# Performance work log

Hardware: AMD Instinct MI355X
Metric: run time of the kernel (lower is better)

## Reference

```python
import jax, jax.numpy as jnp
import numpy as np

H = 4096      # hidden_size
F = 14336     # intermediate_size (ffn)
GS = 64       # HQQ group_size along axis 0 (output rows)
NB = 4        # nbits
T = 512       # tokens routed to this expert


def _make_qlinear(key, N, K):
    """Quantized weight of logical shape (N, K) = (out, in), HQQ axis=0 groups."""
    k1, k2, k3 = jax.random.split(key, 3)
    W_q = jax.random.randint(k1, (N, K), 0, 2 ** NB, dtype=jnp.int32)
    scale = jax.random.uniform(k2, (N // GS, K), dtype=jnp.float32) * 0.02 + 1e-3
    zero = jax.random.uniform(k3, (N // GS, K), dtype=jnp.float32) * (2.0 ** (NB - 1))
    return W_q, scale, zero


def setup_inputs() -> dict:
    key = jax.random.key(0)
    kx, k1, k2, k3 = jax.random.split(key, 4)
    w1_q, w1_scale, w1_zero = _make_qlinear(k1, F, H)  # gate proj
    w2_q, w2_scale, w2_zero = _make_qlinear(k2, H, F)  # down proj
    w3_q, w3_scale, w3_zero = _make_qlinear(k3, F, H)  # up proj
    hidden_states = jax.random.normal(kx, (T, H), dtype=jnp.float32)
    return dict(hidden_states=hidden_states,
                w1_q=w1_q, w1_scale=w1_scale, w1_zero=w1_zero,
                w2_q=w2_q, w2_scale=w2_scale, w2_zero=w2_zero,
                w3_q=w3_q, w3_scale=w3_scale, w3_zero=w3_zero)


def _dequant(W_q, scale, zero):
    # W[n, k] = (W_q[n, k] - zero[n // GS, k]) * scale[n // GS, k]
    N, K = W_q.shape
    Wf = W_q.reshape(N // GS, GS, K).astype(scale.dtype)
    return ((Wf - zero[:, None, :]) * scale[:, None, :]).reshape(N, K)


def reference(hidden_states,
              w1_q, w1_scale, w1_zero,
              w2_q, w2_scale, w2_zero,
              w3_q, w3_scale, w3_zero):
    gate = hidden_states @ _dequant(w1_q, w1_scale, w1_zero).T  # [T, F]
    up = hidden_states @ _dequant(w3_q, w3_scale, w3_zero).T    # [T, F]
    inter = jax.nn.silu(gate) * up                               # [T, F]
    return inter @ _dequant(w2_q, w2_scale, w2_zero).T           # [T, H]
```

## Files before the change

kernel.cpp:

```cpp
#include <hip/hip_runtime.h>
#include <stdint.h>

typedef __bf16 bf16;
typedef __attribute__((ext_vector_type(8))) bf16 bf16x8;
typedef __attribute__((ext_vector_type(4))) bf16 bf16x4;
typedef __attribute__((ext_vector_type(4))) float f32x4;

#define T_DIM 512
#define H_DIM 4096
#define F_DIM 14336

__device__ __forceinline__ int swz(int r, int c) {
    return r * 64 + (c ^ ((r & 7) << 3));
}

__device__ __forceinline__ int xcd_remap(int d, int chunk) {
    return (d & 7) * chunk + (d >> 3);
}

__device__ __forceinline__ void dma16(const void* g, void* l) {
    __builtin_amdgcn_global_load_lds(
        (const __attribute__((address_space(1))) void*)g,
        (__attribute__((address_space(3))) void*)l, 16, 0, 0);
}

#define BARRIER_VM(N)                                                        \
    {                                                                        \
        __builtin_amdgcn_sched_barrier(0);                                   \
        asm volatile("s_waitcnt vmcnt(" #N ") lgkmcnt(0)\n\ts_barrier" ::: "memory"); \
        __builtin_amdgcn_sched_barrier(0);                                   \
    }

__global__ void cvt_x_kernel(const float* __restrict__ x, bf16* __restrict__ xbt) {
    int i = (blockIdx.x * 256 + threadIdx.x) * 4;
    int m = i >> 12;
    int c = i & 4095;
    float4 v = *(const float4*)(x + i);
    bf16x4 o = {(bf16)v.x, (bf16)v.y, (bf16)v.z, (bf16)v.w};
    int p = m >> 7, rm = m & 127, kt = c >> 6, kc = c & 63;
    *(bf16x4*)(xbt + (size_t)(p * 64 + kt) * 8192 + swz(rm, kc)) = o;
}

struct WSet { int4 q1[2], q3[2]; float4 s1, z1, s3, z3; };

__global__ __launch_bounds__(256, 3)
void gemm_gateup(const bf16* __restrict__ A,
                 const int* __restrict__ Wq1, const float* __restrict__ Sc1,
                 const float* __restrict__ Zr1,
                 const int* __restrict__ Wq3, const float* __restrict__ Sc3,
                 const float* __restrict__ Zr3,
                 bf16* __restrict__ inter) {
    constexpr int KD = H_DIM;
    constexpr int NT = KD / 64;
    __shared__ __align__(16) bf16 As[2][128 * 64];
    __shared__ __align__(16) bf16 Bs1[2][32 * 64];
    __shared__ __align__(16) bf16 Bs3[2][32 * 64];

    const int l    = xcd_remap(blockIdx.x, 224);
    const int bx   = l & 3;
    const int by   = l >> 2;
    const int tid  = threadIdx.x;
    const int lane = tid & 63;
    const int wid  = tid >> 6;
    const int wm   = wid >> 1, wn = wid & 1;
    const int lr   = lane & 15;
    const int lk   = (lane >> 4) * 8;
    const int m0   = bx * 128;
    const int n0   = by * 32;
    const int grp  = n0 >> 6;

    const int b_r = (tid >> 4) * 2;
    const int b_c = (tid & 15) * 4;

    const char*  atile = (const char*)A + (size_t)bx * 64 * 16384;
    const size_t dmaoff = (size_t)wid * 4096 + lane * 16;

    const int*   q1B = Wq1 + (size_t)(n0 + b_r) * KD + b_c;
    const int*   q3B = Wq3 + (size_t)(n0 + b_r) * KD + b_c;
    const float* s1B = Sc1 + (size_t)grp * KD + b_c;
    const float* z1B = Zr1 + (size_t)grp * KD + b_c;
    const float* s3B = Sc3 + (size_t)grp * KD + b_c;
    const float* z3B = Zr3 + (size_t)grp * KD + b_c;

    f32x4 acc1[4], acc3[4];
    const f32x4 zf = {0.f, 0.f, 0.f, 0.f};
#pragma unroll
    for (int i = 0; i < 4; i++) { acc1[i] = zf; acc3[i] = zf; }

    WSet sA, sB;

#define GU_DMA(TILE, nb)                                                      \
    {                                                                         \
        const char* _s = atile + (size_t)(TILE) * 16384 + dmaoff;             \
        char* _d = (char*)&As[nb][0] + wid * 4096;                            \
        _Pragma("unroll")                                                     \
        for (int j = 0; j < 4; j++) dma16(_s + j * 1024, _d + j * 1024);      \
    }

#define GU_STAGE(S, K0)                                                       \
    {                                                                         \
        _Pragma("unroll")                                                     \
        for (int i = 0; i < 2; i++) {                                         \
            S.q1[i] = *(const int4*)(q1B + (size_t)i * KD + (K0));            \
            S.q3[i] = *(const int4*)(q3B + (size_t)i * KD + (K0));            \
        }                                                                     \
        S.s1 = *(const float4*)(s1B + (K0));                                  \
        S.z1 = *(const float4*)(z1B + (K0));                                  \
        S.s3 = *(const float4*)(s3B + (K0));                                  \
        S.z3 = *(const float4*)(z3B + (K0));                                  \
    }

#define GU_WLDS(S, nb)                                                        \
    {                                                                         \
        float4 n1, n3;                                                        \
        n1.x = -S.z1.x * S.s1.x; n1.y = -S.z1.y * S.s1.y;                     \
        n1.z = -S.z1.z * S.s1.z; n1.w = -S.z1.w * S.s1.w;                     \
        n3.x = -S.z3.x * S.s3.x; n3.y = -S.z3.y * S.s3.y;                     \
        n3.z = -S.z3.z * S.s3.z; n3.w = -S.z3.w * S.s3.w;                     \
        _Pragma("unroll")                                                     \
        for (int i = 0; i < 2; i++) {                                         \
            bf16x4 v;                                                         \
            v[0] = (bf16)fmaf((float)S.q1[i].x, S.s1.x, n1.x);                \
            v[1] = (bf16)fmaf((float)S.q1[i].y, S.s1.y, n1.y);                \
            v[2] = (bf16)fmaf((float)S.q1[i].z, S.s1.z, n1.z);                \
            v[3] = (bf16)fmaf((float)S.q1[i].w, S.s1.w, n1.w);                \
            *(bf16x4*)&Bs1[nb][swz(b_r + i, b_c)] = v;                        \
            bf16x4 u;                                                         \
            u[0] = (bf16)fmaf((float)S.q3[i].x, S.s3.x, n3.x);                \
            u[1] = (bf16)fmaf((float)S.q3[i].y, S.s3.y, n3.y);                \
            u[2] = (bf16)fmaf((float)S.q3[i].z, S.s3.z, n3.z);                \
            u[3] = (bf16)fmaf((float)S.q3[i].w, S.s3.w, n3.w);                \
            *(bf16x4*)&Bs3[nb][swz(b_r + i, b_c)] = u;                        \
        }                                                                     \
    }

#define GU_MFMA(nb)                                                           \
    {                                                                         \
        _Pragma("unroll")                                                     \
        for (int kk = 0; kk < 2; kk++) {                                      \
            bf16x8 af[4], b1, b3;                                             \
            _Pragma("unroll")                                                 \
            for (int mi = 0; mi < 4; mi++)                                    \
                af[mi] = *(const bf16x8*)&As[nb][swz(wm * 64 + mi * 16 + lr, kk * 32 + lk)]; \
            b1 = *(const bf16x8*)&Bs1[nb][swz(wn * 16 + lr, kk * 32 + lk)];   \
            b3 = *(const bf16x8*)&Bs3[nb][swz(wn * 16 + lr, kk * 32 + lk)];   \
            _Pragma("unroll")                                                 \
            for (int mi = 0; mi < 4; mi++) {                                  \
                acc1[mi] = __builtin_amdgcn_mfma_f32_16x16x32_bf16(af[mi], b1, acc1[mi], 0, 0, 0); \
                acc3[mi] = __builtin_amdgcn_mfma_f32_16x16x32_bf16(af[mi], b3, acc3[mi], 0, 0, 0); \
            }                                                                 \
        }                                                                     \
    }

    GU_STAGE(sA, 0);
    GU_DMA(0, 0);
    GU_WLDS(sA, 0);
    GU_STAGE(sB, 64);
    GU_STAGE(sA, 128);
    BARRIER_VM(16);

    for (int t = 0; t < NT; t += 2) {
        if (t + 1 < NT) GU_DMA(t + 1, 1);
        __builtin_amdgcn_sched_barrier(0);
        GU_MFMA(0);
        if (t + 1 < NT) {
            GU_WLDS(sB, 1);
            if (t + 3 < NT) {
                GU_STAGE(sB, (t + 3) * 64);
                BARRIER_VM(8);
            } else {
                BARRIER_VM(0);
            }
        }
        const int u = t + 1;
        if (u < NT) {
            if (u + 1 < NT) GU_DMA(u + 1, 0);
            __builtin_amdgcn_sched_barrier(0);
            GU_MFMA(1);
            if (u + 1 < NT) {
                GU_WLDS(sA, 0);
                if (u + 3 < NT) {
                    GU_STAGE(sA, (u + 3) * 64);
                    BARRIER_VM(8);
                } else {
                    BARRIER_VM(0);
                }
            }
        }
    }
#undef GU_DMA
#undef GU_STAGE
#undef GU_WLDS
#undef GU_MFMA

    const int orow = (lane >> 4) * 4;
    const int cg   = n0 + wn * 16 + lr;
    const int kt   = cg >> 6, kc = cg & 63;
    bf16* itile = inter + (size_t)(bx * 224 + kt) * 8192;
#pragma unroll
    for (int mi = 0; mi < 4; mi++) {
#pragma unroll
        for (int r = 0; r < 4; r++) {
            int rm = (wm * 64 + mi * 16 + orow + r) & 127;
            float g = acc1[mi][r];
            float u = acc3[mi][r];
            float s = g / (1.0f + __expf(-g));
            itile[swz(rm, kc)] = (bf16)(s * u);
        }
    }
}

struct WSetD { int4 q[2]; float4 s, z; };

template<int SPLITK>
__global__ __launch_bounds__(256, 4)
void gemm_down(const bf16* __restrict__ A,
               const int* __restrict__ Wq,
               const float* __restrict__ Sc, const float* __restrict__ Zr,
               float* __restrict__ partials) {
    constexpr int KD = F_DIM;
    constexpr int KC = KD / SPLITK;
    constexpr int NT = KC / 64;
    __shared__ __align__(16) bf16 As[2][128 * 64];
    __shared__ __align__(16) bf16 Bs[2][32 * 64];

    const int l    = xcd_remap(blockIdx.x, 64 * SPLITK);
    const int bx   = l & 3;
    const int by   = (l >> 2) & 127;
    const int bz   = l >> 9;
    const int tid  = threadIdx.x;
    const int lane = tid & 63;
    const int wid  = tid >> 6;
    const int wm   = wid >> 1, wn = wid & 1;
    const int lr   = lane & 15;
    const int lk   = (lane >> 4) * 8;
    const int m0   = bx * 128;
    const int n0   = by * 32;
    const int grp  = n0 >> 6;
    const int kt0  = bz * (KC / 64);

    const int b_r = (tid >> 4) * 2;
    const int b_c = (tid & 15) * 4;

    const char*  atile = (const char*)A + (size_t)(bx * 224 + kt0) * 16384;
    const size_t dmaoff = (size_t)wid * 4096 + lane * 16;
    const int    kbeg  = bz * KC;

    const int*   qB = Wq + (size_t)(n0 + b_r) * KD + kbeg + b_c;
    const float* sB_ = Sc + (size_t)grp * KD + kbeg + b_c;
    const float* zB_ = Zr + (size_t)grp * KD + kbeg + b_c;

    f32x4 acc[4];
    const f32x4 zf = {0.f, 0.f, 0.f, 0.f};
#pragma unroll
    for (int i = 0; i < 4; i++) acc[i] = zf;

    WSetD sA, sB;

#define GD_DMA(TILE, nb)                                                      \
    {                                                                         \
        const char* _s = atile + (size_t)(TILE) * 16384 + dmaoff;             \
        char* _d = (char*)&As[nb][0] + wid * 4096;                            \
        _Pragma("unroll")                                                     \
        for (int j = 0; j < 4; j++) dma16(_s + j * 1024, _d + j * 1024);      \
    }

#define GD_STAGE(S, K0)                                                       \
    {                                                                         \
        _Pragma("unroll")                                                     \
        for (int i = 0; i < 2; i++)                                           \
            S.q[i] = *(const int4*)(qB + (size_t)i * KD + (K0));              \
        S.s = *(const float4*)(sB_ + (K0));                                   \
        S.z = *(const float4*)(zB_ + (K0));                                   \
    }

#define GD_WLDS(S, nb)                                                        \
    {                                                                         \
        float4 nz;                                                            \
        nz.x = -S.z.x * S.s.x; nz.y = -S.z.y * S.s.y;                         \
        nz.z = -S.z.z * S.s.z; nz.w = -S.z.w * S.s.w;                         \
        _Pragma("unroll")                                                     \
        for (int i = 0; i < 2; i++) {                                         \
            bf16x4 v;                                                         \
            v[0] = (bf16)fmaf((float)S.q[i].x, S.s.x, nz.x);                  \
            v[1] = (bf16)fmaf((float)S.q[i].y, S.s.y, nz.y);                  \
            v[2] = (bf16)fmaf((float)S.q[i].z, S.s.z, nz.z);                  \
            v[3] = (bf16)fmaf((float)S.q[i].w, S.s.w, nz.w);                  \
            *(bf16x4*)&Bs[nb][swz(b_r + i, b_c)] = v;                         \
        }                                                                     \
    }

#define GD_MFMA(nb)                                                           \
    {                                                                         \
        _Pragma("unroll")                                                     \
        for (int kk = 0; kk < 2; kk++) {                                      \
            bf16x8 af[4], bfr;                                                \
            _Pragma("unroll")                                                 \
            for (int mi = 0; mi < 4; mi++)                                    \
                af[mi] = *(const bf16x8*)&As[nb][swz(wm * 64 + mi * 16 + lr, kk * 32 + lk)]; \
            bfr = *(const bf16x8*)&Bs[nb][swz(wn * 16 + lr, kk * 32 + lk)];   \
            _Pragma("unroll")                                                 \
            for (int mi = 0; mi < 4; mi++)                                    \
                acc[mi] = __builtin_amdgcn_mfma_f32_16x16x32_bf16(af[mi], bfr, acc[mi], 0, 0, 0); \
        }                                                                     \
    }

    GD_STAGE(sA, 0);
    GD_DMA(0, 0);
    GD_WLDS(sA, 0);
    GD_STAGE(sB, 64);
    GD_STAGE(sA, 128);
    BARRIER_VM(8);

    for (int t = 0; t < NT; t += 2) {
        if (t + 1 < NT) GD_DMA(t + 1, 1);
        __builtin_amdgcn_sched_barrier(0);
        GD_MFMA(0);
        if (t + 1 < NT) {
            GD_WLDS(sB, 1);
            if (t + 3 < NT) {
                GD_STAGE(sB, (t + 3) * 64);
                BARRIER_VM(4);
            } else {
                BARRIER_VM(0);
            }
        }
        const int u = t + 1;
        if (u < NT) {
            if (u + 1 < NT) GD_DMA(u + 1, 0);
            __builtin_amdgcn_sched_barrier(0);
            GD_MFMA(1);
            if (u + 1 < NT) {
                GD_WLDS(sA, 0);
                if (u + 3 < NT) {
                    GD_STAGE(sA, (u + 3) * 64);
                    BARRIER_VM(4);
                } else {
                    BARRIER_VM(0);
                }
            }
        }
    }
#undef GD_DMA
#undef GD_STAGE
#undef GD_WLDS
#undef GD_MFMA

    float* po = partials + (size_t)bz * T_DIM * H_DIM;
    const int orow = (lane >> 4) * 4;
#pragma unroll
    for (int mi = 0; mi < 4; mi++) {
#pragma unroll
        for (int r = 0; r < 4; r++) {
            int m = m0 + wm * 64 + mi * 16 + orow + r;
            int c = n0 + wn * 16 + lr;
            po[(size_t)m * H_DIM + c] = acc[mi][r];
        }
    }
}

template<int S>
__global__ void reduce_kernel(const float* __restrict__ partials, float* __restrict__ out) {
    size_t i = ((size_t)blockIdx.x * 256 + threadIdx.x) * 4;
    f32x4 a = *(const f32x4*)(partials + i);
#pragma unroll
    for (int s = 1; s < S; s++)
        a += *(const f32x4*)(partials + (size_t)s * T_DIM * H_DIM + i);
    *(f32x4*)(out + i) = a;
}

extern "C" void kernel_launch(void* const* d_in, const int* in_sizes, int n_in,
                              void* d_out, int out_size, void* d_ws, size_t ws_size,
                              hipStream_t stream) {
    const float* x   = (const float*)d_in[0];
    const int*   w1q = (const int*)d_in[1];
    const float* w1s = (const float*)d_in[2];
    const float* w1z = (const float*)d_in[3];
    const int*   w2q = (const int*)d_in[4];
    const float* w2s = (const float*)d_in[5];
    const float* w2z = (const float*)d_in[6];
    const int*   w3q = (const int*)d_in[7];
    const float* w3s = (const float*)d_in[8];
    const float* w3z = (const float*)d_in[9];

    bf16*  xb    = (bf16*)d_ws;
    bf16*  inter = xb + (size_t)T_DIM * H_DIM;
    float* parts = (float*)(inter + (size_t)T_DIM * F_DIM);

    const size_t base   = (size_t)T_DIM * H_DIM * 2 + (size_t)T_DIM * F_DIM * 2;
    const size_t pbytes = (size_t)T_DIM * H_DIM * 4;

    cvt_x_kernel<<<dim3(2048), dim3(256), 0, stream>>>(x, xb);

    gemm_gateup<<<dim3(1792), dim3(256), 0, stream>>>(
        xb, w1q, w1s, w1z, w3q, w3s, w3z, inter);

    if (ws_size >= base + 4 * pbytes) {
        gemm_down<4><<<dim3(2048), dim3(256), 0, stream>>>(inter, w2q, w2s, w2z, parts);
        reduce_kernel<4><<<dim3(2048), dim3(256), 0, stream>>>(parts, (float*)d_out);
    } else if (ws_size >= base + 2 * pbytes) {
        gemm_down<2><<<dim3(1024), dim3(256), 0, stream>>>(inter, w2q, w2s, w2z, parts);
        reduce_kernel<2><<<dim3(2048), dim3(256), 0, stream>>>(parts, (float*)d_out);
    } else {
        gemm_down<1><<<dim3(512), dim3(256), 0, stream>>>(inter, w2q, w2s, w2z, parts);
        reduce_kernel<1><<<dim3(2048), dim3(256), 0, stream>>>(parts, (float*)d_out);
    }
}
```

Baseline: 453.7 us.

## Load gate/up operands directly into registers, dropping LDS staging and barriers

The gate/up GEMM stops staging activations and dequantized weights in shared memory. Each wave now reads its A fragments straight from the pre-swizzled global bf16 tile and dequantizes its own int4 weight fragment in registers, which removes the LDS round trip and the block barriers. Tiles change to a 64x64 N block per block with 16 columns per wave, and launch bounds drop to 2 blocks per SM. In exchange, A is re-read from global/L2 by every wave with no sharing, register pressure rises, and occupancy falls.

```diff
diff --git a/kernel.cpp b/kernel.cpp
--- a/kernel.cpp
+++ b/kernel.cpp
@@ -30,6 +30,20 @@
         asm volatile("s_waitcnt vmcnt(" #N ") lgkmcnt(0)\n\ts_barrier" ::: "memory"); \
         __builtin_amdgcn_sched_barrier(0);                                   \
     }
+
+__device__ __forceinline__ bf16x8 deq8(int4 qa, int4 qb, float4 sa, float4 sb,
+                                       float4 za, float4 zb) {
+    bf16x8 r;
+    r[0] = (bf16)(((float)qa.x - za.x) * sa.x);
+    r[1] = (bf16)(((float)qa.y - za.y) * sa.y);
+    r[2] = (bf16)(((float)qa.z - za.z) * sa.z);
+    r[3] = (bf16)(((float)qa.w - za.w) * sa.w);
+    r[4] = (bf16)(((float)qb.x - zb.x) * sb.x);
+    r[5] = (bf16)(((float)qb.y - zb.y) * sb.y);
+    r[6] = (bf16)(((float)qb.z - zb.z) * sb.z);
+    r[7] = (bf16)(((float)qb.w - zb.w) * sb.w);
+    return r;
+}
 
 __global__ void cvt_x_kernel(const float* __restrict__ x, bf16* __restrict__ xbt) {
     int i = (blockIdx.x * 256 + threadIdx.x) * 4;
@@ -41,9 +55,9 @@
     *(bf16x4*)(xbt + (size_t)(p * 64 + kt) * 8192 + swz(rm, kc)) = o;
 }
 
-struct WSet { int4 q1[2], q3[2]; float4 s1, z1, s3, z3; };
-
-__global__ __launch_bounds__(256, 3)
+struct QSet { int4 q1[4], q3[4]; };
+
+__global__ __launch_bounds__(256, 2)
 void gemm_gateup(const bf16* __restrict__ A,
                  const int* __restrict__ Wq1, const float* __restrict__ Sc1,
                  const float* __restrict__ Zr1,
@@ -52,160 +66,121 @@
                  bf16* __restrict__ inter) {
     constexpr int KD = H_DIM;
     constexpr int NT = KD / 64;
-    __shared__ __align__(16) bf16 As[2][128 * 64];
-    __shared__ __align__(16) bf16 Bs1[2][32 * 64];
-    __shared__ __align__(16) bf16 Bs3[2][32 * 64];
 
     const int l    = xcd_remap(blockIdx.x, 224);
-    const int bx   = l & 3;
-    const int by   = l >> 2;
+    const int mp   = l & 7;
+    const int np   = l >> 3;
     const int tid  = threadIdx.x;
     const int lane = tid & 63;
-    const int wid  = tid >> 6;
-    const int wm   = wid >> 1, wn = wid & 1;
+    const int w    = tid >> 6;
     const int lr   = lane & 15;
     const int lk   = (lane >> 4) * 8;
-    const int m0   = bx * 128;
-    const int n0   = by * 32;
-    const int grp  = n0 >> 6;
-
-    const int b_r = (tid >> 4) * 2;
-    const int b_c = (tid & 15) * 4;
-
-    const char*  atile = (const char*)A + (size_t)bx * 64 * 16384;
-    const size_t dmaoff = (size_t)wid * 4096 + lane * 16;
-
-    const int*   q1B = Wq1 + (size_t)(n0 + b_r) * KD + b_c;
-    const int*   q3B = Wq3 + (size_t)(n0 + b_r) * KD + b_c;
-    const float* s1B = Sc1 + (size_t)grp * KD + b_c;
-    const float* z1B = Zr1 + (size_t)grp * KD + b_c;
-    const float* s3B = Sc3 + (size_t)grp * KD + b_c;
-    const float* z3B = Zr3 + (size_t)grp * KD + b_c;
+    const int n0   = np * 64 + w * 16;
+    const int rowW = n0 + lr;
+
+    const bf16* at0 = A + (size_t)(mp >> 1) * 64 * 8192;
+    const int   rmb = (mp & 1) * 64;
+
+    int aoff[4][2];
+#pragma unroll
+    for (int mi = 0; mi < 4; mi++)
+#pragma unroll
+        for (int kk = 0; kk < 2; kk++)
+            aoff[mi][kk] = swz(rmb + mi * 16 + lr, kk * 32 + lk);
+
+    const int*   q1B = Wq1 + (size_t)rowW * KD + lk;
+    const int*   q3B = Wq3 + (size_t)rowW * KD + lk;
+    const float* s1B = Sc1 + (size_t)np * KD + lk;
+    const float* z1B = Zr1 + (size_t)np * KD + lk;
+    const float* s3B = Sc3 + (size_t)np * KD + lk;
+    const float* z3B = Zr3 + (size_t)np * KD + lk;
 
     f32x4 acc1[4], acc3[4];
     const f32x4 zf = {0.f, 0.f, 0.f, 0.f};
 #pragma unroll
     for (int i = 0; i < 4; i++) { acc1[i] = zf; acc3[i] = zf; }
 
-    WSet sA, sB;
-
-#define GU_DMA(TILE, nb)                                                      \
-    {                                                                         \
-        const char* _s = atile + (size_t)(TILE) * 16384 + dmaoff;             \
-        char* _d = (char*)&As[nb][0] + wid * 4096;                            \
-        _Pragma("unroll")                                                     \
-        for (int j = 0; j < 4; j++) dma16(_s + j * 1024, _d + j * 1024);      \
-    }
-
-#define GU_STAGE(S, K0)                                                       \
-    {                                                                         \
-        _Pragma("unroll")                                                     \
-        for (int i = 0; i < 2; i++) {                                         \
-            S.q1[i] = *(const int4*)(q1B + (size_t)i * KD + (K0));            \
-            S.q3[i] = *(const int4*)(q3B + (size_t)i * KD + (K0));            \
+    QSet  qa, qb;
+    float4 s1[4], z1[4], s3[4], z3[4];
+
+#define QST(S, K0)                                                            \
+    {                                                                         \
+        _Pragma("unroll")                                                     \
+        for (int kk = 0; kk < 2; kk++)                                        \
+            _Pragma("unroll")                                                 \
+            for (int h = 0; h < 2; h++) {                                     \
+                S.q1[kk * 2 + h] = *(const int4*)(q1B + (K0) + kk * 32 + h * 4); \
+                S.q3[kk * 2 + h] = *(const int4*)(q3B + (K0) + kk * 32 + h * 4); \
+            }                                                                 \
+    }
+
+#define SZST(K0)                                                              \
+    {                                                                         \
+        _Pragma("unroll")                                                     \
+        for (int kk = 0; kk < 2; kk++)                                        \
+            _Pragma("unroll")                                                 \
+            for (int h = 0; h < 2; h++) {                                     \
+                int o = (K0) + kk * 32 + h * 4;                               \
+                s1[kk * 2 + h] = *(const float4*)(s1B + o);                   \
+                z1[kk * 2 + h] = *(const float4*)(z1B + o);                   \
+                s3[kk * 2 + h] = *(const float4*)(s3B + o);                   \
+                z3[kk * 2 + h] = *(const float4*)(z3B + o);                   \
+            }                                                                 \
+    }
+
+#define BODY(S, T)                                                            \
+    {                                                                         \
+        const bf16* at = at0 + (size_t)(T) * 8192;                            \
+        bf16x8 a_[4][2];                                                      \
+        _Pragma("unroll")                                                     \
+        for (int mi = 0; mi < 4; mi++)                                        \
+            _Pragma("unroll")                                                 \
+            for (int kk = 0; kk < 2; kk++)                                    \
+                a_[mi][kk] = *(const bf16x8*)(at + aoff[mi][kk]);             \
+        bf16x8 b1f[2], b3f[2];                                                \
+        _Pragma("unroll")                                                     \
+        for (int kk = 0; kk < 2; kk++) {                                      \
+            b1f[kk] = deq8(S.q1[kk * 2], S.q1[kk * 2 + 1], s1[kk * 2],        \
+                           s1[kk * 2 + 1], z1[kk * 2], z1[kk * 2 + 1]);       \
+            b3f[kk] = deq8(S.q3[kk * 2], S.q3[kk * 2 + 1], s3[kk * 2],        \
+                           s3[kk * 2 + 1], z3[kk * 2], z3[kk * 2 + 1]);       \
         }                                                                     \
-        S.s1 = *(const float4*)(s1B + (K0));                                  \
-        S.z1 = *(const float4*)(z1B + (K0));                                  \
-        S.s3 = *(const float4*)(s3B + (K0));                                  \
-        S.z3 = *(const float4*)(z3B + (K0));                                  \
-    }
-
-#define GU_WLDS(S, nb)                                                        \
-    {                                                                         \
-        float4 n1, n3;                                                        \
-        n1.x = -S.z1.x * S.s1.x; n1.y = -S.z1.y * S.s1.y;                     \
-        n1.z = -S.z1.z * S.s1.z; n1.w = -S.z1.w * S.s1.w;                     \
-        n3.x = -S.z3.x * S.s3.x; n3.y = -S.z3.y * S.s3.y;                     \
-        n3.z = -S.z3.z * S.s3.z; n3.w = -S.z3.w * S.s3.w;                     \
-        _Pragma("unroll")                                                     \
-        for (int i = 0; i < 2; i++) {                                         \
-            bf16x4 v;                                                         \
-            v[0] = (bf16)fmaf((float)S.q1[i].x, S.s1.x, n1.x);                \
-            v[1] = (bf16)fmaf((float)S.q1[i].y, S.s1.y, n1.y);                \
-            v[2] = (bf16)fmaf((float)S.q1[i].z, S.s1.z, n1.z);                \
-            v[3] = (bf16)fmaf((float)S.q1[i].w, S.s1.w, n1.w);                \
-            *(bf16x4*)&Bs1[nb][swz(b_r + i, b_c)] = v;                        \
-            bf16x4 u;                                                         \
-            u[0] = (bf16)fmaf((float)S.q3[i].x, S.s3.x, n3.x);                \
-            u[1] = (bf16)fmaf((float)S.q3[i].y, S.s3.y, n3.y);                \
-            u[2] = (bf16)fmaf((float)S.q3[i].z, S.s3.z, n3.z);                \
-            u[3] = (bf16)fmaf((float)S.q3[i].w, S.s3.w, n3.w);                \
-            *(bf16x4*)&Bs3[nb][swz(b_r + i, b_c)] = u;                        \
-        }                                                                     \
-    }
-
-#define GU_MFMA(nb)                                                           \
-    {                                                                         \
-        _Pragma("unroll")                                                     \
-        for (int kk = 0; kk < 2; kk++) {                                      \
-            bf16x8 af[4], b1, b3;                                             \
-            _Pragma("unroll")                                                 \
-            for (int mi = 0; mi < 4; mi++)                                    \
-                af[mi] = *(const bf16x8*)&As[nb][swz(wm * 64 + mi * 16 + lr, kk * 32 + lk)]; \
-            b1 = *(const bf16x8*)&Bs1[nb][swz(wn * 16 + lr, kk * 32 + lk)];   \
-            b3 = *(const bf16x8*)&Bs3[nb][swz(wn * 16 + lr, kk * 32 + lk)];   \
+        if ((T) + 2 < NT) QST(S, ((T) + 2) * 64);                             \
+        if ((T) + 1 < NT) SZST(((T) + 1) * 64);                               \
+        _Pragma("unroll")                                                     \
+        for (int kk = 0; kk < 2; kk++)                                        \
             _Pragma("unroll")                                                 \
             for (int mi = 0; mi < 4; mi++) {                                  \
-                acc1[mi] = __builtin_amdgcn_mfma_f32_16x16x32_bf16(af[mi], b1, acc1[mi], 0, 0, 0); \
-                acc3[mi] = __builtin_amdgcn_mfma_f32_16x16x32_bf16(af[mi], b3, acc3[mi], 0, 0, 0); \
+                acc1[mi] = __builtin_amdgcn_mfma_f32_16x16x32_bf16(a_[mi][kk], b1f[kk], acc1[mi], 0, 0, 0); \
+                acc3[mi] = __builtin_amdgcn_mfma_f32_16x16x32_bf16(a_[mi][kk], b3f[kk], acc3[mi], 0, 0, 0); \
             }                                                                 \
-        }                                                                     \
-    }
-
-    GU_STAGE(sA, 0);
-    GU_DMA(0, 0);
-    GU_WLDS(sA, 0);
-    GU_STAGE(sB, 64);
-    GU_STAGE(sA, 128);
-    BARRIER_VM(16);
+    }
+
+    QST(qa, 0);
+    QST(qb, 64);
+    SZST(0);
 
     for (int t = 0; t < NT; t += 2) {
-        if (t + 1 < NT) GU_DMA(t + 1, 1);
-        __builtin_amdgcn_sched_barrier(0);
-        GU_MFMA(0);
-        if (t + 1 < NT) {
-            GU_WLDS(sB, 1);
-            if (t + 3 < NT) {
-                GU_STAGE(sB, (t + 3) * 64);
-                BARRIER_VM(8);
-            } else {
-                BARRIER_VM(0);
-            }
-        }
-        const int u = t + 1;
-        if (u < NT) {
-            if (u + 1 < NT) GU_DMA(u + 1, 0);
-            __builtin_amdgcn_sched_barrier(0);
-            GU_MFMA(1);
-            if (u + 1 < NT) {
-                GU_WLDS(sA, 0);
-                if (u + 3 < NT) {
-                    GU_STAGE(sA, (u + 3) * 64);
-                    BARRIER_VM(8);
-                } else {
-                    BARRIER_VM(0);
-                }
-            }
-        }
-    }
-#undef GU_DMA
-#undef GU_STAGE
-#undef GU_WLDS
-#undef GU_MFMA
+        BODY(qa, t);
+        BODY(qb, t + 1);
+    }
+#undef QST
+#undef SZST
+#undef BODY
 
     const int orow = (lane >> 4) * 4;
-    const int cg   = n0 + wn * 16 + lr;
+    const int cg   = n0 + lr;
     const int kt   = cg >> 6, kc = cg & 63;
-    bf16* itile = inter + (size_t)(bx * 224 + kt) * 8192;
+    bf16* itile = inter + (size_t)((mp >> 1) * 224 + kt) * 8192;
 #pragma unroll
     for (int mi = 0; mi < 4; mi++) {
 #pragma unroll
         for (int r = 0; r < 4; r++) {
-            int rm = (wm * 64 + mi * 16 + orow + r) & 127;
+            int rm2 = rmb + mi * 16 + orow + r;
             float g = acc1[mi][r];
             float u = acc3[mi][r];
             float s = g / (1.0f + __expf(-g));
-            itile[swz(rm, kc)] = (bf16)(s * u);
+            itile[swz(rm2, kc)] = (bf16)(s * u);
         }
     }
 }
@@ -246,7 +221,7 @@
     const size_t dmaoff = (size_t)wid * 4096 + lane * 16;
     const int    kbeg  = bz * KC;
 
-    const int*   qB = Wq + (size_t)(n0 + b_r) * KD + kbeg + b_c;
+    const int*   qB  = Wq + (size_t)(n0 + b_r) * KD + kbeg + b_c;
     const float* sB_ = Sc + (size_t)grp * KD + kbeg + b_c;
     const float* zB_ = Zr + (size_t)grp * KD + kbeg + b_c;
 
```

Result: slower. 1.552 ms (+242.0%).

## Read activation tiles directly from global memory instead of staging through LDS

Applied to the files above, without the earlier changes.

Both GEMM kernels stop copying the pre-swizzled bf16 activation tile into shared memory with global_load_lds and instead have each lane load its A fragments straight from global or L2 at precomputed swizzled offsets. Only the dequantised weight tiles stay double-buffered in LDS. The barrier no longer waits on vmcnt. Scale and zero loads are split from the quantised-weight prefetch into one set of registers. Gate/up launch bounds rise to 4 blocks per SM because LDS use drops. This removes LDS traffic and the DMA waits for A, but exposes MFMA operands to global-load latency, and the redundant A reads across N-blocks now go through cache.

```diff
diff --git a/kernel.cpp b/kernel.cpp
--- a/kernel.cpp
+++ b/kernel.cpp
@@ -18,18 +18,11 @@
     return (d & 7) * chunk + (d >> 3);
 }
 
-__device__ __forceinline__ void dma16(const void* g, void* l) {
-    __builtin_amdgcn_global_load_lds(
-        (const __attribute__((address_space(1))) void*)g,
-        (__attribute__((address_space(3))) void*)l, 16, 0, 0);
-}
-
-#define BARRIER_VM(N)                                                        \
-    {                                                                        \
-        __builtin_amdgcn_sched_barrier(0);                                   \
-        asm volatile("s_waitcnt vmcnt(" #N ") lgkmcnt(0)\n\ts_barrier" ::: "memory"); \
-        __builtin_amdgcn_sched_barrier(0);                                   \
-    }
+__device__ __forceinline__ void barrier_nodrain() {
+    __builtin_amdgcn_sched_barrier(0);
+    asm volatile("s_waitcnt lgkmcnt(0)\n\ts_barrier" ::: "memory");
+    __builtin_amdgcn_sched_barrier(0);
+}
 
 __global__ void cvt_x_kernel(const float* __restrict__ x, bf16* __restrict__ xbt) {
     int i = (blockIdx.x * 256 + threadIdx.x) * 4;
@@ -41,9 +34,9 @@
     *(bf16x4*)(xbt + (size_t)(p * 64 + kt) * 8192 + swz(rm, kc)) = o;
 }
 
-struct WSet { int4 q1[2], q3[2]; float4 s1, z1, s3, z3; };
-
-__global__ __launch_bounds__(256, 3)
+struct QSet { int4 q1[2], q3[2]; };
+
+__global__ __launch_bounds__(256, 4)
 void gemm_gateup(const bf16* __restrict__ A,
                  const int* __restrict__ Wq1, const float* __restrict__ Sc1,
                  const float* __restrict__ Zr1,
@@ -52,7 +45,6 @@
                  bf16* __restrict__ inter) {
     constexpr int KD = H_DIM;
     constexpr int NT = KD / 64;
-    __shared__ __align__(16) bf16 As[2][128 * 64];
     __shared__ __align__(16) bf16 Bs1[2][32 * 64];
     __shared__ __align__(16) bf16 Bs3[2][32 * 64];
 
@@ -65,15 +57,20 @@
     const int wm   = wid >> 1, wn = wid & 1;
     const int lr   = lane & 15;
     const int lk   = (lane >> 4) * 8;
-    const int m0   = bx * 128;
     const int n0   = by * 32;
     const int grp  = n0 >> 6;
 
     const int b_r = (tid >> 4) * 2;
     const int b_c = (tid & 15) * 4;
 
-    const char*  atile = (const char*)A + (size_t)bx * 64 * 16384;
-    const size_t dmaoff = (size_t)wid * 4096 + lane * 16;
+    const bf16* at0 = A + (size_t)bx * 64 * 8192;
+
+    int aoff[4][2];
+#pragma unroll
+    for (int mi = 0; mi < 4; mi++)
+#pragma unroll
+        for (int kk = 0; kk < 2; kk++)
+            aoff[mi][kk] = swz(wm * 64 + mi * 16 + lr, kk * 32 + lk);
 
     const int*   q1B = Wq1 + (size_t)(n0 + b_r) * KD + b_c;
     const int*   q3B = Wq3 + (size_t)(n0 + b_r) * KD + b_c;
@@ -87,111 +84,94 @@
 #pragma unroll
     for (int i = 0; i < 4; i++) { acc1[i] = zf; acc3[i] = zf; }
 
-    WSet sA, sB;
-
-#define GU_DMA(TILE, nb)                                                      \
-    {                                                                         \
-        const char* _s = atile + (size_t)(TILE) * 16384 + dmaoff;             \
-        char* _d = (char*)&As[nb][0] + wid * 4096;                            \
-        _Pragma("unroll")                                                     \
-        for (int j = 0; j < 4; j++) dma16(_s + j * 1024, _d + j * 1024);      \
-    }
-
-#define GU_STAGE(S, K0)                                                       \
+    QSet qa, qb;
+    float4 s1r, z1r, s3r, z3r;
+
+#define QST(S, K0)                                                            \
     {                                                                         \
         _Pragma("unroll")                                                     \
         for (int i = 0; i < 2; i++) {                                         \
             S.q1[i] = *(const int4*)(q1B + (size_t)i * KD + (K0));            \
             S.q3[i] = *(const int4*)(q3B + (size_t)i * KD + (K0));            \
         }                                                                     \
-        S.s1 = *(const float4*)(s1B + (K0));                                  \
-        S.z1 = *(const float4*)(z1B + (K0));                                  \
-        S.s3 = *(const float4*)(s3B + (K0));                                  \
-        S.z3 = *(const float4*)(z3B + (K0));                                  \
-    }
-
-#define GU_WLDS(S, nb)                                                        \
+    }
+
+#define SZST(K0)                                                              \
+    {                                                                         \
+        s1r = *(const float4*)(s1B + (K0));                                   \
+        z1r = *(const float4*)(z1B + (K0));                                   \
+        s3r = *(const float4*)(s3B + (K0));                                   \
+        z3r = *(const float4*)(z3B + (K0));                                   \
+    }
+
+#define WLDS(S, nb)                                                           \
     {                                                                         \
         float4 n1, n3;                                                        \
-        n1.x = -S.z1.x * S.s1.x; n1.y = -S.z1.y * S.s1.y;                     \
-        n1.z = -S.z1.z * S.s1.z; n1.w = -S.z1.w * S.s1.w;                     \
-        n3.x = -S.z3.x * S.s3.x; n3.y = -S.z3.y * S.s3.y;                     \
-        n3.z = -S.z3.z * S.s3.z; n3.w = -S.z3.w * S.s3.w;                     \
+        n1.x = -z1r.x * s1r.x; n1.y = -z1r.y * s1r.y;                         \
+        n1.z = -z1r.z * s1r.z; n1.w = -z1r.w * s1r.w;                         \
+        n3.x = -z3r.x * s3r.x; n3.y = -z3r.y * s3r.y;                         \
+        n3.z = -z3r.z * s3r.z; n3.w = -z3r.w * s3r.w;                         \
         _Pragma("unroll")                                                     \
         for (int i = 0; i < 2; i++) {                                         \
             bf16x4 v;                                                         \
-            v[0] = (bf16)fmaf((float)S.q1[i].x, S.s1.x, n1.x);                \
-            v[1] = (bf16)fmaf((float)S.q1[i].y, S.s1.y, n1.y);                \
-            v[2] = (bf16)fmaf((float)S.q1[i].z, S.s1.z, n1.z);                \
-            v[3] = (bf16)fmaf((float)S.q1[i].w, S.s1.w, n1.w);                \
+            v[0] = (bf16)fmaf((float)S.q1[i].x, s1r.x, n1.x);                 \
+            v[1] = (bf16)fmaf((float)S.q1[i].y, s1r.y, n1.y);                 \
+            v[2] = (bf16)fmaf((float)S.q1[i].z, s1r.z, n1.z);                 \
+            v[3] = (bf16)fmaf((float)S.q1[i].w, s1r.w, n1.w);                 \
             *(bf16x4*)&Bs1[nb][swz(b_r + i, b_c)] = v;                        \
             bf16x4 u;                                                         \
-            u[0] = (bf16)fmaf((float)S.q3[i].x, S.s3.x, n3.x);                \
-            u[1] = (bf16)fmaf((float)S.q3[i].y, S.s3.y, n3.y);                \
-            u[2] = (bf16)fmaf((float)S.q3[i].z, S.s3.z, n3.z);                \
-            u[3] = (bf16)fmaf((float)S.q3[i].w, S.s3.w, n3.w);                \
+            u[0] = (bf16)fmaf((float)S.q3[i].x, s3r.x, n3.x);                 \
+            u[1] = (bf16)fmaf((float)S.q3[i].y, s3r.y, n3.y);                 \
+            u[2] = (bf16)fmaf((float)S.q3[i].z, s3r.z, n3.z);                 \
+            u[3] = (bf16)fmaf((float)S.q3[i].w, s3r.w, n3.w);                 \
             *(bf16x4*)&Bs3[nb][swz(b_r + i, b_c)] = u;                        \
         }                                                                     \
     }
 
-#define GU_MFMA(nb)                                                           \
-    {                                                                         \
+#define GU_STEP(T, QS)                                                        \
+    {                                                                         \
+        const bf16* at = at0 + (size_t)(T) * 8192;                            \
         _Pragma("unroll")                                                     \
         for (int kk = 0; kk < 2; kk++) {                                      \
-            bf16x8 af[4], b1, b3;                                             \
-            _Pragma("unroll")                                                 \
-            for (int mi = 0; mi < 4; mi++)                                    \
-                af[mi] = *(const bf16x8*)&As[nb][swz(wm * 64 + mi * 16 + lr, kk * 32 + lk)]; \
-            b1 = *(const bf16x8*)&Bs1[nb][swz(wn * 16 + lr, kk * 32 + lk)];   \
-            b3 = *(const bf16x8*)&Bs3[nb][swz(wn * 16 + lr, kk * 32 + lk)];   \
-            _Pragma("unroll")                                                 \
-            for (int mi = 0; mi < 4; mi++) {                                  \
-                acc1[mi] = __builtin_amdgcn_mfma_f32_16x16x32_bf16(af[mi], b1, acc1[mi], 0, 0, 0); \
-                acc3[mi] = __builtin_amdgcn_mfma_f32_16x16x32_bf16(af[mi], b3, acc3[mi], 0, 0, 0); \
-            }                                                                 \
-        }                                                                     \
-    }
-
-    GU_STAGE(sA, 0);
-    GU_DMA(0, 0);
-    GU_WLDS(sA, 0);
-    GU_STAGE(sB, 64);
-    GU_STAGE(sA, 128);
-    BARRIER_VM(16);
+            bf16x8 a0 = *(const bf16x8*)(at + aoff[0][kk]);                   \
+            bf16x8 a1 = *(const bf16x8*)(at + aoff[1][kk]);                   \
+            bf16x8 a2 = *(const bf16x8*)(at + aoff[2][kk]);                   \
+            bf16x8 a3 = *(const bf16x8*)(at + aoff[3][kk]);                   \
+            bf16x8 b1 = *(const bf16x8*)&Bs1[(T) & 1][swz(wn * 16 + lr, kk * 32 + lk)]; \
+            bf16x8 b3 = *(const bf16x8*)&Bs3[(T) & 1][swz(wn * 16 + lr, kk * 32 + lk)]; \
+            acc1[0] = __builtin_amdgcn_mfma_f32_16x16x32_bf16(a0, b1, acc1[0], 0, 0, 0); \
+            acc3[0] = __builtin_amdgcn_mfma_f32_16x16x32_bf16(a0, b3, acc3[0], 0, 0, 0); \
+            acc1[1] = __builtin_amdgcn_mfma_f32_16x16x32_bf16(a1, b1, acc1[1], 0, 0, 0); \
+            acc3[1] = __builtin_amdgcn_mfma_f32_16x16x32_bf16(a1, b3, acc3[1], 0, 0, 0); \
+            acc1[2] = __builtin_amdgcn_mfma_f32_16x16x32_bf16(a2, b1, acc1[2], 0, 0, 0); \
+            acc3[2] = __builtin_amdgcn_mfma_f32_16x16x32_bf16(a2, b3, acc3[2], 0, 0, 0); \
+            acc1[3] = __builtin_amdgcn_mfma_f32_16x16x32_bf16(a3, b1, acc1[3], 0, 0, 0); \
+            acc3[3] = __builtin_amdgcn_mfma_f32_16x16x32_bf16(a3, b3, acc3[3], 0, 0, 0); \
+        }                                                                     \
+        if ((T) + 1 < NT) {                                                   \
+            WLDS(QS, ((T) + 1) & 1);                                          \
+            if ((T) + 3 < NT) QST(QS, ((T) + 3) * 64);                        \
+            if ((T) + 2 < NT) SZST(((T) + 2) * 64);                           \
+            barrier_nodrain();                                                \
+        }                                                                     \
+    }
+
+    QST(qa, 0);
+    SZST(0);
+    WLDS(qa, 0);
+    QST(qa, 64);
+    QST(qb, 128);
+    SZST(64);
+    barrier_nodrain();
 
     for (int t = 0; t < NT; t += 2) {
-        if (t + 1 < NT) GU_DMA(t + 1, 1);
-        __builtin_amdgcn_sched_barrier(0);
-        GU_MFMA(0);
-        if (t + 1 < NT) {
-            GU_WLDS(sB, 1);
-            if (t + 3 < NT) {
-                GU_STAGE(sB, (t + 3) * 64);
-                BARRIER_VM(8);
-            } else {
-                BARRIER_VM(0);
-            }
-        }
-        const int u = t + 1;
-        if (u < NT) {
-            if (u + 1 < NT) GU_DMA(u + 1, 0);
-            __builtin_amdgcn_sched_barrier(0);
-            GU_MFMA(1);
-            if (u + 1 < NT) {
-                GU_WLDS(sA, 0);
-                if (u + 3 < NT) {
-                    GU_STAGE(sA, (u + 3) * 64);
-                    BARRIER_VM(8);
-                } else {
-                    BARRIER_VM(0);
-                }
-            }
-        }
-    }
-#undef GU_DMA
-#undef GU_STAGE
-#undef GU_WLDS
-#undef GU_MFMA
+        GU_STEP(t, qa);
+        GU_STEP(t + 1, qb);
+    }
+#undef QST
+#undef SZST
+#undef WLDS
+#undef GU_STEP
 
     const int orow = (lane >> 4) * 4;
     const int cg   = n0 + wn * 16 + lr;
@@ -201,7 +181,7 @@
     for (int mi = 0; mi < 4; mi++) {
 #pragma unroll
         for (int r = 0; r < 4; r++) {
-            int rm = (wm * 64 + mi * 16 + orow + r) & 127;
+            int rm = wm * 64 + mi * 16 + orow + r;
             float g = acc1[mi][r];
             float u = acc3[mi][r];
             float s = g / (1.0f + __expf(-g));
@@ -210,7 +190,7 @@
     }
 }
 
-struct WSetD { int4 q[2]; float4 s, z; };
+struct QSetD { int4 q[2]; };
 
 template<int SPLITK>
 __global__ __launch_bounds__(256, 4)
@@ -221,7 +201,6 @@
     constexpr int KD = F_DIM;
     constexpr int KC = KD / SPLITK;
     constexpr int NT = KC / 64;
-    __shared__ __align__(16) bf16 As[2][128 * 64];
     __shared__ __align__(16) bf16 Bs[2][32 * 64];
 
     const int l    = xcd_remap(blockIdx.x, 64 * SPLITK);
@@ -238,15 +217,21 @@
     const int n0   = by * 32;
     const int grp  = n0 >> 6;
     const int kt0  = bz * (KC / 64);
+    const int kbeg = bz * KC;
 
     const int b_r = (tid >> 4) * 2;
     const int b_c = (tid & 15) * 4;
 
-    const char*  atile = (const char*)A + (size_t)(bx * 224 + kt0) * 16384;
-    const size_t dmaoff = (size_t)wid * 4096 + lane * 16;
-    const int    kbeg  = bz * KC;
-
-    const int*   qB = Wq + (size_t)(n0 + b_r) * KD + kbeg + b_c;
+    const bf16* at0 = A + (size_t)(bx * 224 + kt0) * 8192;
+
+    int aoff[4][2];
+#pragma unroll
+    for (int mi = 0; mi < 4; mi++)
+#pragma unroll
+        for (int kk = 0; kk < 2; kk++)
+            aoff[mi][kk] = swz(wm * 64 + mi * 16 + lr, kk * 32 + lk);
+
+    const int*   qB  = Wq + (size_t)(n0 + b_r) * KD + kbeg + b_c;
     const float* sB_ = Sc + (size_t)grp * KD + kbeg + b_c;
     const float* zB_ = Zr + (size_t)grp * KD + kbeg + b_c;
 
@@ -255,96 +240,77 @@
 #pragma unroll
     for (int i = 0; i < 4; i++) acc[i] = zf;
 
-    WSetD sA, sB;
-
-#define GD_DMA(TILE, nb)                                                      \
-    {                                                                         \
-        const char* _s = atile + (size_t)(TILE) * 16384 + dmaoff;             \
-        char* _d = (char*)&As[nb][0] + wid * 4096;                            \
-        _Pragma("unroll")                                                     \
-        for (int j = 0; j < 4; j++) dma16(_s + j * 1024, _d + j * 1024);      \
-    }
-
-#define GD_STAGE(S, K0)                                                       \
+    QSetD qa, qb;
+    float4 sr, zr;
+
+#define QST(S, K0)                                                            \
     {                                                                         \
         _Pragma("unroll")                                                     \
         for (int i = 0; i < 2; i++)                                           \
             S.q[i] = *(const int4*)(qB + (size_t)i * KD + (K0));              \
-        S.s = *(const float4*)(sB_ + (K0));                                   \
-        S.z = *(const float4*)(zB_ + (K0));                                   \
-    }
-
-#define GD_WLDS(S, nb)                                                        \
+    }
+
+#define SZST(K0)                                                              \
+    {                                                                         \
+        sr = *(const float4*)(sB_ + (K0));                                    \
+        zr = *(const float4*)(zB_ + (K0));                                    \
+    }
+
+#define WLDS(S, nb)                                                           \
     {                                                                         \
         float4 nz;                                                            \
-        nz.x = -S.z.x * S.s.x; nz.y = -S.z.y * S.s.y;                         \
-        nz.z = -S.z.z * S.s.z; nz.w = -S.z.w * S.s.w;                         \
+        nz.x = -zr.x * sr.x; nz.y = -zr.y * sr.y;                             \
+        nz.z = -zr.z * sr.z; nz.w = -zr.w * sr.w;                             \
         _Pragma("unroll")                                                     \
         for (int i = 0; i < 2; i++) {                                         \
             bf16x4 v;                                                         \
-            v[0] = (bf16)fmaf((float)S.q[i].x, S.s.x, nz.x);                  \
-            v[1] = (bf16)fmaf((float)S.q[i].y, S.s.y, nz.y);                  \
-            v[2] = (bf16)fmaf((float)S.q[i].z, S.s.z, nz.z);                  \
-            v[3] = (bf16)fmaf((float)S.q[i].w, S.s.w, nz.w);                  \
+            v[0] = (bf16)fmaf((float)S.q[i].x, sr.x, nz.x);                   \
+            v[1] = (bf16)fmaf((float)S.q[i].y, sr.y, nz.y);                   \
+            v[2] = (bf16)fmaf((float)S.q[i].z, sr.z, nz.z);                   \
+            v[3] = (bf16)fmaf((float)S.q[i].w, sr.w, nz.w);                   \
             *(bf16x4*)&Bs[nb][swz(b_r + i, b_c)] = v;                         \
         }                                                                     \
     }
 
-#define GD_MFMA(nb)                                                           \
-    {                                                                         \
+#define GD_STEP(T, QS)                                                        \
+    {                                                                         \
+        const bf16* at = at0 + (size_t)(T) * 8192;                            \
         _Pragma("unroll")                                                     \
         for (int kk = 0; kk < 2; kk++) {                                      \
-            bf16x8 af[4], bfr;                                                \
-            _Pragma("unroll")                                                 \
-            for (int mi = 0; mi < 4; mi++)                                    \
-                af[mi] = *(const bf16x8*)&As[nb][swz(wm * 64 + mi * 16 + lr, kk * 32 + lk)]; \
-            bfr = *(const bf16x8*)&Bs[nb][swz(wn * 16 + lr, kk * 32 + lk)];   \
-            _Pragma("unroll")                                                 \
-            for (int mi = 0; mi < 4; mi++)                                    \
-                acc[mi] = __builtin_amdgcn_mfma_f32_16x16x32_bf16(af[mi], bfr, acc[mi], 0, 0, 0); \
-        }                                                                     \
-    }
-
-    GD_STAGE(sA, 0);
-    GD_DMA(0, 0);
-    GD_WLDS(sA, 0);
-    GD_STAGE(sB, 64);
-    GD_STAGE(sA, 128);
-    BARRIER_VM(8);
+            bf16x8 a0 = *(const bf16x8*)(at + aoff[0][kk]);                   \
+            bf16x8 a1 = *(const bf16x8*)(at + aoff[1][kk]);                   \
+            bf16x8 a2 = *(const bf16x8*)(at + aoff[2][kk]);                   \
+            bf16x8 a3 = *(const bf16x8*)(at + aoff[3][kk]);                   \
+            bf16x8 bv = *(const bf16x8*)&Bs[(T) & 1][swz(wn * 16 + lr, kk * 32 + lk)]; \
+            acc[0] = __builtin_amdgcn_mfma_f32_16x16x32_bf16(a0, bv, acc[0], 0, 0, 0); \
+            acc[1] = __builtin_amdgcn_mfma_f32_16x16x32_bf16(a1, bv, acc[1], 0, 0, 0); \
+            acc[2] = __builtin_amdgcn_mfma_f32_16x16x32_bf16(a2, bv, acc[2], 0, 0, 0); \
+            acc[3] = __builtin_amdgcn_mfma_f32_16x16x32_bf16(a3, bv, acc[3], 0, 0, 0); \
+        }                                                                     \
+        if ((T) + 1 < NT) {                                                   \
+            WLDS(QS, ((T) + 1) & 1);                                          \
+            if ((T) + 3 < NT) QST(QS, ((T) + 3) * 64);                        \
+            if ((T) + 2 < NT) SZST(((T) + 2) * 64);                           \
+            barrier_nodrain();                                                \
+        }                                                                     \
+    }
+
+    QST(qa, 0);
+    SZST(0);
+    WLDS(qa, 0);
+    QST(qa, 64);
+    QST(qb, 128);
+    SZST(64);
+    barrier_nodrain();
 
     for (int t = 0; t < NT; t += 2) {
-        if (t + 1 < NT) GD_DMA(t + 1, 1);
-        __builtin_amdgcn_sched_barrier(0);
-        GD_MFMA(0);
-        if (t + 1 < NT) {
-            GD_WLDS(sB, 1);
-            if (t + 3 < NT) {
-                GD_STAGE(sB, (t + 3) * 64);
-                BARRIER_VM(4);
-            } else {
-                BARRIER_VM(0);
-            }
-        }
-        const int u = t + 1;
-        if (u < NT) {
-            if (u + 1 < NT) GD_DMA(u + 1, 0);
-            __builtin_amdgcn_sched_barrier(0);
-            GD_MFMA(1);
-            if (u + 1 < NT) {
-                GD_WLDS(sA, 0);
-                if (u + 3 < NT) {
-                    GD_STAGE(sA, (u + 3) * 64);
-                    BARRIER_VM(4);
-                } else {
-                    BARRIER_VM(0);
-                }
-            }
-        }
-    }
-#undef GD_DMA
-#undef GD_STAGE
-#undef GD_WLDS
-#undef GD_MFMA
+        GD_STEP(t, qa);
+        GD_STEP(t + 1, qb);
+    }
+#undef QST
+#undef SZST
+#undef WLDS
+#undef GD_STEP
 
     float* po = partials + (size_t)bz * T_DIM * H_DIM;
     const int orow = (lane >> 4) * 4;
```

New measurement: 1.307 ms. 188% more time.
